# Kernel optimization log

Measured on AMD Instinct MI355X. Metric: run time of the kernel, lower is better.

The kernel has to match this reference:

```python
import jax, jax.numpy as jnp
import numpy as np

SIGMA = 1.0
SQRT2 = float(np.sqrt(2.0))


def setup_inputs() -> dict:
    key = jax.random.key(0)
    k1, k2 = jax.random.split(key)
    B, L = 128, 1024
    preds = jax.random.normal(k1, (B, L), dtype=jnp.float32)
    # integer relevance grades 0..4, stored as float as in the torch module
    target = jax.random.randint(k2, (B, L), 0, 5).astype(jnp.float32)
    return {"preds": preds, "target": target}


def reference(preds, target):
    B, L = preds.shape
    # pairwise diff [B, L, L]: diff[b,i,j] = preds[b,i] - preds[b,j]
    diff = preds[:, :, None] - preds[:, None, :]
    # Normal(0, sigma*sqrt(2)).cdf(diff) == ndtr(diff / (sigma*sqrt(2)))
    p = jax.scipy.special.ndtr(diff / (SIGMA * SQRT2))
    # zero the diagonal (i == j) before summing
    eye = jnp.eye(L, dtype=bool)
    p = jnp.where(eye[None, :, :], 0.0, p)
    expected_ranks = 1.0 + p.sum(axis=2)  # [B, L]

    gains = 2.0 ** target - 1.0
    discounts = jnp.log2(expected_ranks + 1.0)
    dcg = (gains / discounts).sum(axis=1)  # [B]

    ideal_target = jnp.sort(target, axis=1)[:, ::-1]  # descending
    ideal_gains = 2.0 ** ideal_target - 1.0
    ideal_discounts = jnp.log2(jnp.arange(1, L + 1, dtype=jnp.float32) + 1.0)
    idcg = (ideal_gains / ideal_discounts).sum(axis=1)  # [B]

    ndcg = dcg / (idcg + 1e-10)
    return -ndcg.mean()
```

## Files before the change

kernel.cpp:

```cpp
#include <hip/hip_runtime.h>

#define B 128
#define L 1024

#if __has_builtin(__builtin_amdgcn_exp2f)
#define EXP2(x) __builtin_amdgcn_exp2f(x)
#else
#define EXP2(x) __expf((x) * 0.6931471805599453f)
#endif


__global__ __launch_bounds__(256) void init_ws(float* ws) {
    int t = threadIdx.x;
    ws[t] = 0.0f;
    if (t < 2) ws[256 + t] = 0.0f;
}

#define K1 -1.6279072f
#define K2 -0.9299637f
#define K3 -0.1074808f

__device__ __forceinline__ float phi_term(float pi, float pj) {
    float d = pi - pj;
    float a = __builtin_fabsf(d);
    float t = __builtin_fmaf(K3, a, K2);
    float u = __builtin_fmaf(t, a, K1);
    float e = EXP2(a * u);
    return __builtin_copysignf(1.0f - e, d);
}

__global__ __launch_bounds__(256) void pair_fused_kernel(const float* __restrict__ preds,
                                                         const float* __restrict__ target,
                                                         float* __restrict__ ws,
                                                         float* __restrict__ out) {
    __shared__ float sp[L];
    __shared__ float wred[4];
    __shared__ int lastflag;
    __shared__ unsigned long long cred[256];
    __shared__ float fred[256];

    const int b    = blockIdx.x >> 2;
    const int iseg = blockIdx.x & 3;
    const int tid  = threadIdx.x;
    const float* prow = preds + b * L;
    const float* trow = target + b * L;

    float4 v4 = reinterpret_cast<const float4*>(prow)[tid];
    v4.x *= 0.5f; v4.y *= 0.5f; v4.z *= 0.5f; v4.w *= 0.5f;
    reinterpret_cast<float4*>(sp)[tid] = v4;

    const int i = iseg * 256 + tid;
    const float tgt = trow[i];

    __syncthreads();

    const float pi = sp[i];

    float a0 = 0.f, a1 = 0.f, a2 = 0.f, a3 = 0.f,
          a4 = 0.f, a5 = 0.f, a6 = 0.f, a7 = 0.f;
    for (int j = 0; j < L; j += 8) {
        float4 va = *reinterpret_cast<const float4*>(&sp[j]);
        float4 vb = *reinterpret_cast<const float4*>(&sp[j + 4]);
        a0 += phi_term(pi, va.x);
        a1 += phi_term(pi, va.y);
        a2 += phi_term(pi, va.z);
        a3 += phi_term(pi, va.w);
        a4 += phi_term(pi, vb.x);
        a5 += phi_term(pi, vb.y);
        a6 += phi_term(pi, vb.z);
        a7 += phi_term(pi, vb.w);
    }
    float E = ((a0 + a1) + (a2 + a3)) + ((a4 + a5) + (a6 + a7));
    float er1 = 513.5f + 0.5f * E;

    float g = EXP2(tgt) - 1.0f;
    float contrib = g * __builtin_amdgcn_rcpf(__log2f(er1));

    #pragma unroll
    for (int off = 32; off > 0; off >>= 1)
        contrib += __shfl_down(contrib, off);
    if ((tid & 63) == 0) wred[tid >> 6] = contrib;
    __syncthreads();

    if (tid == 0) {
        float blocksum = (wred[0] + wred[1]) + (wred[2] + wred[3]);
        atomicAdd(&ws[b], blocksum);
        __threadfence();
        int old = atomicAdd((int*)ws + 128 + b, 1);
        lastflag = (old == 3);
    }
    __syncthreads();

    if (!lastflag) return;

    unsigned long long cnt = 0ull;
    #pragma unroll
    for (int k = 0; k < 4; ++k) {
        float t = trow[tid + k * 256];
        cnt += ((unsigned long long)(t > 3.5f) << 48)
             + ((unsigned long long)(t > 2.5f) << 32)
             + ((unsigned long long)(t > 1.5f) << 16)
             + ((unsigned long long)(t > 0.5f));
    }
    cred[tid] = cnt;
    __syncthreads();
    #pragma unroll
    for (int s = 128; s > 0; s >>= 1) {
        if (tid < (unsigned)s) cred[tid] += cred[tid + s];
        __syncthreads();
    }
    unsigned long long tot = cred[0];
    const int n4 = (int)(tot >> 48) & 0xFFFF;
    const int n3 = (int)(tot >> 32) & 0xFFFF;
    const int n2 = (int)(tot >> 16) & 0xFFFF;
    const int n1 = (int)(tot)       & 0xFFFF;

    float idcg_p = 0.0f;
    #pragma unroll
    for (int k = 0; k < 4; ++k) {
        int pos = tid + 1 + k * 256;
        float gain = (pos <= n4) ? 15.0f : (pos <= n3) ? 7.0f :
                     (pos <= n2) ? 3.0f  : (pos <= n1) ? 1.0f : 0.0f;
        idcg_p += gain * __builtin_amdgcn_rcpf(__log2f((float)pos + 1.0f));
    }
    fred[tid] = idcg_p;
    __syncthreads();
    #pragma unroll
    for (int s = 128; s > 0; s >>= 1) {
        if (tid < (unsigned)s) fred[tid] += fred[tid + s];
        __syncthreads();
    }

    if (tid == 0) {
        __threadfence();
        float dcgv = atomicAdd(&ws[b], 0.0f);
        float ndcg = dcgv / (fred[0] + 1e-10f);
        atomicAdd(&ws[256], ndcg);
        __threadfence();
        int old2 = atomicAdd((int*)ws + 257, 1);
        if (old2 == B - 1) {
            float acc = atomicAdd(&ws[256], 0.0f);
            out[0] = -acc * (1.0f / (float)B);
        }
    }
}

extern "C" void kernel_launch(void* const* d_in, const int* in_sizes, int n_in,
                              void* d_out, int out_size, void* d_ws, size_t ws_size,
                              hipStream_t stream) {
    const float* preds  = (const float*)d_in[0];
    const float* target = (const float*)d_in[1];
    float* out = (float*)d_out;
    float* ws  = (float*)d_ws;

    init_ws<<<1, 256, 0, stream>>>(ws);
    pair_fused_kernel<<<B * 4, 256, 0, stream>>>(preds, target, ws, out);
}
```

Measured before the change: 95.67 us.

## Split pairwise j-range across blocks and reduce partial ranks in last block

```diff
diff --git a/kernel.cpp b/kernel.cpp
--- a/kernel.cpp
+++ b/kernel.cpp
@@ -9,18 +9,21 @@
 #define EXP2(x) __expf((x) * 0.6931471805599453f)
 #endif
 
+#define WS_E    0
+#define WS_CTR  524288
+#define WS_ACC  524416
+#define WS_GCTR 524417
 
 __global__ __launch_bounds__(256) void init_ws(float* ws) {
     int t = threadIdx.x;
-    ws[t] = 0.0f;
-    if (t < 2) ws[256 + t] = 0.0f;
+    if (t < 130) ws[WS_CTR + t] = 0.0f;
 }
 
 #define K1 -1.6279072f
 #define K2 -0.9299637f
 #define K3 -0.1074808f
 
-__device__ __forceinline__ float phi_term(float pi, float pj) {
+__device__ __forceinline__ float erf_term(float pi, float pj) {
     float d = pi - pj;
     float a = __builtin_fabsf(d);
     float t = __builtin_fmaf(K3, a, K2);
@@ -29,74 +32,77 @@
     return __builtin_copysignf(1.0f - e, d);
 }
 
-__global__ __launch_bounds__(256) void pair_fused_kernel(const float* __restrict__ preds,
-                                                         const float* __restrict__ target,
-                                                         float* __restrict__ ws,
-                                                         float* __restrict__ out) {
-    __shared__ float sp[L];
-    __shared__ float wred[4];
+__global__ __launch_bounds__(256, 8) void pair_kernel(const float* __restrict__ preds,
+                                                      const float* __restrict__ target,
+                                                      float* __restrict__ ws,
+                                                      float* __restrict__ out) {
+    __shared__ float sj[256];
+    __shared__ float wdummy; (void)wdummy;
+    __shared__ unsigned long long cred[256];
+    __shared__ float2 fred[256];
     __shared__ int lastflag;
-    __shared__ unsigned long long cred[256];
-    __shared__ float fred[256];
 
-    const int b    = blockIdx.x >> 2;
-    const int iseg = blockIdx.x & 3;
+    const int blk  = blockIdx.x;
+    const int b    = blk >> 4;
+    const int iseg = (blk >> 2) & 3;
+    const int jseg = blk & 3;
     const int tid  = threadIdx.x;
+
     const float* prow = preds + b * L;
-    const float* trow = target + b * L;
 
-    float4 v4 = reinterpret_cast<const float4*>(prow)[tid];
-    v4.x *= 0.5f; v4.y *= 0.5f; v4.z *= 0.5f; v4.w *= 0.5f;
-    reinterpret_cast<float4*>(sp)[tid] = v4;
-
-    const int i = iseg * 256 + tid;
-    const float tgt = trow[i];
-
+    if (tid < 64) {
+        float4 v = reinterpret_cast<const float4*>(prow + jseg * 256)[tid];
+        v.x *= 0.5f; v.y *= 0.5f; v.z *= 0.5f; v.w *= 0.5f;
+        reinterpret_cast<float4*>(sj)[tid] = v;
+    }
+    const int i  = iseg * 256 + tid;
+    const float pi = 0.5f * prow[i];
     __syncthreads();
-
-    const float pi = sp[i];
 
     float a0 = 0.f, a1 = 0.f, a2 = 0.f, a3 = 0.f,
           a4 = 0.f, a5 = 0.f, a6 = 0.f, a7 = 0.f;
-    for (int j = 0; j < L; j += 8) {
-        float4 va = *reinterpret_cast<const float4*>(&sp[j]);
-        float4 vb = *reinterpret_cast<const float4*>(&sp[j + 4]);
-        a0 += phi_term(pi, va.x);
-        a1 += phi_term(pi, va.y);
-        a2 += phi_term(pi, va.z);
-        a3 += phi_term(pi, va.w);
-        a4 += phi_term(pi, vb.x);
-        a5 += phi_term(pi, vb.y);
-        a6 += phi_term(pi, vb.z);
-        a7 += phi_term(pi, vb.w);
+    for (int j = 0; j < 256; j += 8) {
+        float4 va = *reinterpret_cast<const float4*>(&sj[j]);
+        float4 vb = *reinterpret_cast<const float4*>(&sj[j + 4]);
+        a0 += erf_term(pi, va.x);
+        a1 += erf_term(pi, va.y);
+        a2 += erf_term(pi, va.z);
+        a3 += erf_term(pi, va.w);
+        a4 += erf_term(pi, vb.x);
+        a5 += erf_term(pi, vb.y);
+        a6 += erf_term(pi, vb.z);
+        a7 += erf_term(pi, vb.w);
     }
     float E = ((a0 + a1) + (a2 + a3)) + ((a4 + a5) + (a6 + a7));
-    float er1 = 513.5f + 0.5f * E;
 
-    float g = EXP2(tgt) - 1.0f;
-    float contrib = g * __builtin_amdgcn_rcpf(__log2f(er1));
-
-    #pragma unroll
-    for (int off = 32; off > 0; off >>= 1)
-        contrib += __shfl_down(contrib, off);
-    if ((tid & 63) == 0) wred[tid >> 6] = contrib;
+    __hip_atomic_store(&ws[WS_E + jseg * (B * L) + b * L + i], E,
+                       __ATOMIC_RELAXED, __HIP_MEMORY_SCOPE_AGENT);
+    __threadfence();
     __syncthreads();
-
     if (tid == 0) {
-        float blocksum = (wred[0] + wred[1]) + (wred[2] + wred[3]);
-        atomicAdd(&ws[b], blocksum);
-        __threadfence();
-        int old = atomicAdd((int*)ws + 128 + b, 1);
-        lastflag = (old == 3);
+        int old = atomicAdd((int*)ws + WS_CTR + b, 1);
+        lastflag = (old == 15);
     }
     __syncthreads();
-
     if (!lastflag) return;
 
+    __threadfence();
+    const float* trow = target + b * L;
+
+    float dcg_p = 0.0f;
     unsigned long long cnt = 0ull;
     #pragma unroll
     for (int k = 0; k < 4; ++k) {
-        float t = trow[tid + k * 256];
+        int ii = tid + k * 256;
+        float Es = 0.0f;
+        #pragma unroll
+        for (int js = 0; js < 4; ++js)
+            Es += __hip_atomic_load(&ws[WS_E + js * (B * L) + b * L + ii],
+                                    __ATOMIC_RELAXED, __HIP_MEMORY_SCOPE_AGENT);
+        float er1 = 513.5f + 0.5f * Es;
+        float t = trow[ii];
+        float g = EXP2(t) - 1.0f;
+        dcg_p += g * __builtin_amdgcn_rcpf(__log2f(er1));
         cnt += ((unsigned long long)(t > 3.5f) << 48)
              + ((unsigned long long)(t > 2.5f) << 32)
              + ((unsigned long long)(t > 1.5f) << 16)
@@ -123,23 +129,26 @@
                      (pos <= n2) ? 3.0f  : (pos <= n1) ? 1.0f : 0.0f;
         idcg_p += gain * __builtin_amdgcn_rcpf(__log2f((float)pos + 1.0f));
     }
-    fred[tid] = idcg_p;
+    fred[tid] = make_float2(dcg_p, idcg_p);
     __syncthreads();
     #pragma unroll
     for (int s = 128; s > 0; s >>= 1) {
-        if (tid < (unsigned)s) fred[tid] += fred[tid + s];
+        if (tid < (unsigned)s) {
+            float2 x = fred[tid], y = fred[tid + s];
+            fred[tid] = make_float2(x.x + y.x, x.y + y.y);
+        }
         __syncthreads();
     }
 
     if (tid == 0) {
+        float ndcg = fred[0].x / (fred[0].y + 1e-10f);
+        atomicAdd(&ws[WS_ACC], ndcg);
         __threadfence();
-        float dcgv = atomicAdd(&ws[b], 0.0f);
-        float ndcg = dcgv / (fred[0] + 1e-10f);
-        atomicAdd(&ws[256], ndcg);
-        __threadfence();
-        int old2 = atomicAdd((int*)ws + 257, 1);
+        int old2 = atomicAdd((int*)ws + WS_GCTR, 1);
         if (old2 == B - 1) {
-            float acc = atomicAdd(&ws[256], 0.0f);
+            __threadfence();
+            float acc = __hip_atomic_load(&ws[WS_ACC], __ATOMIC_RELAXED,
+                                          __HIP_MEMORY_SCOPE_AGENT);
             out[0] = -acc * (1.0f / (float)B);
         }
     }
@@ -154,5 +163,5 @@
     float* ws  = (float*)d_ws;
 
     init_ws<<<1, 256, 0, stream>>>(ws);
-    pair_fused_kernel<<<B * 4, 256, 0, stream>>>(preds, target, ws, out);
+    pair_kernel<<<B * 16, 256, 0, stream>>>(preds, target, ws, out);
 }
```

New measurement: 222.9 us. +133.0%, slower.
